# Performance work log

Measured on AMD Instinct MI355X. Metric: run time of the kernel, lower is better.

## Reference

```python
import jax, jax.numpy as jnp
import numpy as np

B, S, DIM, H = 2, 2048, 2048, 16
HD = DIM // H  # 128
ROPE_THETA = 10000.0
NEG = -1e9


def setup_inputs() -> dict:
    key = jax.random.key(0)
    ks = jax.random.split(key, 6)
    x = jax.random.normal(ks[0], (B, S, DIM), dtype=jnp.float32)
    # rotary embedding tables: angle[s, j] = s / theta^(2j/HD), j in [0, HD/2)
    inv_freq = 1.0 / (ROPE_THETA ** (jnp.arange(0, HD, 2, dtype=jnp.float32) / HD))
    angles = jnp.arange(S, dtype=jnp.float32)[:, None] * inv_freq[None, :]  # (S, HD/2)
    freqs_cos = jnp.cos(angles)
    freqs_sin = jnp.sin(angles)
    # causal additive mask (1,1,S,S)
    causal = jnp.tril(jnp.ones((S, S), dtype=jnp.bool_))
    mask = jnp.where(causal, 0.0, NEG).astype(jnp.float32)[None, None]
    sc = 1.0 / np.sqrt(DIM)
    wq = jax.random.normal(ks[1], (DIM, DIM), dtype=jnp.float32) * sc
    wk = jax.random.normal(ks[2], (DIM, DIM), dtype=jnp.float32) * sc
    wv = jax.random.normal(ks[3], (DIM, DIM), dtype=jnp.float32) * sc
    wo = jax.random.normal(ks[4], (DIM, DIM), dtype=jnp.float32) * sc
    return {"x": x, "freqs_cos": freqs_cos, "freqs_sin": freqs_sin,
            "mask": mask, "wq": wq, "wk": wk, "wv": wv, "wo": wo}


def _apply_rope(t, cos, sin):
    # t: (B,S,H,HD); cos/sin: (S, HD/2) -> broadcast (1,S,1,HD/2)
    tr = t[..., ::2]
    ti = t[..., 1::2]
    c = cos[None, :, None, :]
    s = sin[None, :, None, :]
    out_r = tr * c - ti * s
    out_i = tr * s + ti * c
    # interleave back: stack on last axis then flatten -> [r0,i0,r1,i1,...]
    return jnp.stack([out_r, out_i], axis=-1).reshape(t.shape)


def reference(x, freqs_cos, freqs_sin, mask, wq, wk, wv, wo):
    b, s, _ = x.shape
    xq = (x @ wq).reshape(b, s, H, HD)
    xk = (x @ wk).reshape(b, s, H, HD)
    xv = (x @ wv).reshape(b, s, H, HD)
    xq = _apply_rope(xq, freqs_cos, freqs_sin)
    xk = _apply_rope(xk, freqs_cos, freqs_sin)
    # (B,H,S,HD)
    q = jnp.transpose(xq, (0, 2, 1, 3)) * (1.0 / np.sqrt(HD))
    k = jnp.transpose(xk, (0, 2, 1, 3))
    v = jnp.transpose(xv, (0, 2, 1, 3))
    attn = jnp.einsum('bhqd,bhkd->bhqk', q, k) + mask[:, :, :s, :s]
    attn = jax.nn.softmax(attn, axis=-1)
    out = jnp.einsum('bhqk,bhkd->bhqd', attn, v)  # (B,H,S,HD)
    out = jnp.transpose(out, (0, 2, 1, 3)).reshape(b, s, H * HD)
    return out @ wo
```

## Files before the change

kernel.cpp:

```cpp
#include <hip/hip_runtime.h>
#include <hip/hip_bf16.h>
#include <cstdint>
#include <cstddef>

#define BB   2
#define SS   2048
#define DD   2048
#define HH   16
#define HDD  128
#define SEC  8388608

typedef unsigned short u16;
typedef __attribute__((ext_vector_type(8))) short short8;
typedef __attribute__((ext_vector_type(4))) float f32x4;

__device__ __forceinline__ u16 f2bf(float f) {
  union { float f; uint32_t u; } v; v.f = f;
  uint32_t r = v.u + 0x7fffu + ((v.u >> 16) & 1u);
  return (u16)(r >> 16);
}
__device__ __forceinline__ float bf2f(u16 b) {
  union { uint32_t u; float f; } v; v.u = ((uint32_t)b) << 16;
  return v.f;
}

__device__ __forceinline__ void gload16(const u16* g, u16* l) {
  __builtin_amdgcn_global_load_lds(
      (__attribute__((address_space(1))) void*)g,
      (__attribute__((address_space(3))) void*)l, 16, 0, 0);
}

__global__ void k_prep(const float* __restrict__ x,
                       const float* __restrict__ w0, const float* __restrict__ w1,
                       const float* __restrict__ w2, const float* __restrict__ w3,
                       u16* __restrict__ xb, u16* __restrict__ wt) {
  const int z = blockIdx.z;
  if (z == 4) {
    const int id = blockIdx.y * 64 + blockIdx.x;
    const int t = threadIdx.y * 32 + threadIdx.x;
    const size_t base = ((size_t)id * 256 + t) * 2;
    const float4* xv = reinterpret_cast<const float4*>(x);
    uint2* ov = reinterpret_cast<uint2*>(xb);
#pragma unroll
    for (int u = 0; u < 2; ++u) {
      const float4 v = xv[base + u];
      uint2 p;
      p.x = (uint32_t)f2bf(v.x) | ((uint32_t)f2bf(v.y) << 16);
      p.y = (uint32_t)f2bf(v.z) | ((uint32_t)f2bf(v.w) << 16);
      ov[base + u] = p;
    }
    return;
  }
  __shared__ float tls[32][33];
  const float* w = (z == 0) ? w0 : (z == 1) ? w1 : (z == 2) ? w2 : w3;
  u16* o = wt + (size_t)z * (DD * DD);
  const int n0 = blockIdx.x * 32, k0 = blockIdx.y * 32;
  const int tx = threadIdx.x, ty = threadIdx.y;
#pragma unroll
  for (int i = 0; i < 32; i += 8)
    tls[ty + i][tx] = w[(size_t)(k0 + ty + i) * DD + n0 + tx];
  __syncthreads();
#pragma unroll
  for (int i = 0; i < 32; i += 8)
    o[(size_t)(n0 + ty + i) * DD + k0 + tx] = f2bf(tls[tx][ty + i]);
}

template <int MODE>
__global__ __launch_bounds__(256) void k_gemm(const u16* __restrict__ A,
                                              const u16* __restrict__ Bt,
                                              void* __restrict__ out,
                                              const float* __restrict__ fc,
                                              const float* __restrict__ fs) {
  __shared__ __align__(16) u16 As[128 * 32];
  __shared__ __align__(16) u16 Bs[128 * 32];
  const int tid = threadIdx.x;
  const int wave = tid >> 6, lane = tid & 63;
  const int c = lane & 15, g = lane >> 4;
  const int row0 = blockIdx.x * 128, col0 = blockIdx.y * 128;
  const int wm = wave >> 1, wn = wave & 1;
  const int sr = lane >> 2;
  const int sk = (lane & 3) * 8;
  f32x4 acc[4][4] = {};
  for (int k0 = 0; k0 < DD; k0 += 32) {
#pragma unroll
    for (int r = 0; r < 2; ++r) {
      const int chunk = r * 4 + wave;
      const int row = chunk * 16 + sr;
      gload16(A  + (size_t)(row0 + row) * DD + k0 + sk, As + chunk * 512);
      gload16(Bt + (size_t)(col0 + row) * DD + k0 + sk, Bs + chunk * 512);
    }
    __syncthreads();
    short8 a[4], b[4];
#pragma unroll
    for (int i = 0; i < 4; ++i)
      a[i] = *reinterpret_cast<const short8*>(As + (wm * 64 + i * 16 + c) * 32 + g * 8);
#pragma unroll
    for (int j = 0; j < 4; ++j)
      b[j] = *reinterpret_cast<const short8*>(Bs + (wn * 64 + j * 16 + c) * 32 + g * 8);
#pragma unroll
    for (int i = 0; i < 4; ++i)
#pragma unroll
      for (int j = 0; j < 4; ++j)
        acc[i][j] = __builtin_amdgcn_mfma_f32_16x16x32_bf16(a[i], b[j], acc[i][j], 0, 0, 0);
    __syncthreads();
  }
  if (MODE == 0) {
    const int which = col0 >> 11;
    u16* o16 = reinterpret_cast<u16*>(out);
#pragma unroll
    for (int i = 0; i < 4; ++i) {
#pragma unroll
      for (int j = 0; j < 4; ++j) {
        const int mb = row0 + wm * 64 + i * 16 + g * 4;
        const int n  = col0 + wn * 64 + j * 16 + c;
        const int h_ = (n >> 7) & 15, d_ = n & (HDD - 1);
        const int b_ = mb >> 11, s0_ = mb & (SS - 1);
        if (which == 2) {
          ushort4 pk;
          pk.x = f2bf(acc[i][j][0]); pk.y = f2bf(acc[i][j][1]);
          pk.z = f2bf(acc[i][j][2]); pk.w = f2bf(acc[i][j][3]);
          *reinterpret_cast<ushort4*>(
              o16 + 2 * (size_t)SEC + (((size_t)(b_ * HH + h_)) * HDD + d_) * SS + s0_) = pk;
        } else {
          const int p = d_ >> 1;
          const bool ev = (d_ & 1) == 0;
          const float qsc = (which == 0) ? 0.08838834764831845f : 1.0f;
#pragma unroll
          for (int r = 0; r < 4; ++r) {
            const int s_ = s0_ + r;
            const float own = acc[i][j][r];
            const float par = __shfl_xor(own, 1);
            const float cv = fc[s_ * 64 + p], sv = fs[s_ * 64 + p];
            const float ro = ev ? (own * cv - par * sv) : (par * sv + own * cv);
            o16[(size_t)which * SEC + (((size_t)(b_ * HH + h_)) * SS + s_) * HDD + d_] =
                f2bf(ro * qsc);
          }
        }
      }
    }
  } else {
#pragma unroll
    for (int i = 0; i < 4; ++i) {
#pragma unroll
      for (int j = 0; j < 4; ++j) {
        const int mb = row0 + wm * 64 + i * 16 + g * 4;
        const int n  = col0 + wn * 64 + j * 16 + c;
#pragma unroll
        for (int r = 0; r < 4; ++r)
          reinterpret_cast<float*>(out)[(size_t)(mb + r) * DD + n] = acc[i][j][r];
      }
    }
  }
}

__global__ __launch_bounds__(256, 3) void k_attn(const u16* __restrict__ Q,
                                                 const u16* __restrict__ K,
                                                 const u16* __restrict__ Vt,
                                                 u16* __restrict__ O) {
  __shared__ __align__(16) u16 Kt[2][32 * 128];
  __shared__ __align__(16) u16 Vs[2][128 * 32];
  __shared__ __align__(16) u16 Pb[4 * 32 * 40];
  const int tid = threadIdx.x;
  const int wave = tid >> 6, lane = tid & 63;
  const int c = lane & 15, g = lane >> 4;
  const int l = blockIdx.x;
  int qi, bh;
  if (l < 256) { qi = 8 + (l & 7); bh = l >> 3; }
  else         { qi = 7 - ((l - 256) & 7); bh = (l - 256) >> 3; }
  const int q0 = qi * 128;
  const u16* Qp = Q  + (size_t)bh * SS * HDD;
  const u16* Kp = K  + (size_t)bh * SS * HDD;
  const u16* Vp = Vt + (size_t)bh * SS * HDD;
  short8 qf[2][4];
#pragma unroll
  for (int ms = 0; ms < 2; ++ms)
#pragma unroll
    for (int kd = 0; kd < 4; ++kd)
      qf[ms][kd] = *reinterpret_cast<const short8*>(
          Qp + (size_t)(q0 + wave * 32 + ms * 16 + c) * HDD + kd * 32 + g * 8);
  f32x4 acc[2][8] = {};
  float psum[2][4] = {};
  const int ntiles = (qi + 1) * 4;
  u16* pwav = Pb + wave * (32 * 40);
  const int krl = lane >> 4, kcl = lane & 15;
  const int vrl = lane >> 2, vcl = lane & 3;
  auto stage = [&](int t) {
    const int kv0 = t * 32;
    u16* kb = Kt[t & 1];
    u16* vb = Vs[t & 1];
#pragma unroll
    for (int j = 0; j < 2; ++j) {
      const int r0k = (j * 4 + wave) * 4;
      const int rowk = r0k + krl;
      gload16(Kp + (size_t)(kv0 + rowk) * HDD + ((kcl ^ (rowk & 15)) << 3),
              kb + r0k * 128);
      const int r0v = (j * 4 + wave) * 16;
      const int rowv = r0v + vrl;
      gload16(Vp + (size_t)rowv * SS + kv0 + ((vcl ^ (vrl & 3)) << 3),
              vb + r0v * 32);
    }
  };
  stage(0);
  for (int t = 0; t < ntiles; ++t) {
    __syncthreads();
    if (t + 1 < ntiles) stage(t + 1);
    const int kv0 = t * 32;
    const bool active = kv0 <= q0 + wave * 32 + 31;
    if (!active) continue;
    const u16* kb = Kt[t & 1];
    const u16* vv = Vs[t & 1];
    f32x4 s[2][2] = {};
#pragma unroll
    for (int ns = 0; ns < 2; ++ns)
#pragma unroll
      for (int kd = 0; kd < 4; ++kd) {
        const short8 b = *reinterpret_cast<const short8*>(
            kb + (ns * 16 + c) * 128 + (((kd * 4 + g) ^ c) << 3));
        s[0][ns] = __builtin_amdgcn_mfma_f32_16x16x32_bf16(qf[0][kd], b, s[0][ns], 0, 0, 0);
        s[1][ns] = __builtin_amdgcn_mfma_f32_16x16x32_bf16(qf[1][kd], b, s[1][ns], 0, 0, 0);
      }
#pragma unroll
    for (int ms = 0; ms < 2; ++ms) {
      const int qrow = q0 + wave * 32 + ms * 16 + g * 4;
#pragma unroll
      for (int r = 0; r < 4; ++r) {
        u16* pw = pwav + (ms * 16 + g * 4 + r) * 40 + c;
        float rs = 0.f;
#pragma unroll
        for (int ns = 0; ns < 2; ++ns) {
          const bool u = (kv0 + ns * 16 + c) <= (qrow + r);
          const float p = u ? __expf(s[ms][ns][r]) : 0.f;
          rs += p;
          pw[ns * 16] = f2bf(p);
        }
        psum[ms][r] += rs;
      }
    }
    short8 pa[2];
    pa[0] = *reinterpret_cast<const short8*>(pwav + c * 40 + g * 8);
    pa[1] = *reinterpret_cast<const short8*>(pwav + (16 + c) * 40 + g * 8);
#pragma unroll
    for (int nb = 0; nb < 8; ++nb) {
      const short8 vb2 = *reinterpret_cast<const short8*>(
          vv + (nb * 16 + c) * 32 + ((g ^ (c & 3)) << 3));
      acc[0][nb] = __builtin_amdgcn_mfma_f32_16x16x32_bf16(pa[0], vb2, acc[0][nb], 0, 0, 0);
      acc[1][nb] = __builtin_amdgcn_mfma_f32_16x16x32_bf16(pa[1], vb2, acc[1][nb], 0, 0, 0);
    }
  }
  const int b_ = bh >> 4, h_ = bh & 15;
#pragma unroll
  for (int ms = 0; ms < 2; ++ms) {
#pragma unroll
    for (int r = 0; r < 4; ++r) {
      float rs = psum[ms][r];
      rs += __shfl_xor(rs, 1);
      rs += __shfl_xor(rs, 2);
      rs += __shfl_xor(rs, 4);
      rs += __shfl_xor(rs, 8);
      const float inv = 1.f / rs;
      const int s_ = q0 + wave * 32 + ms * 16 + g * 4 + r;
      u16* op = O + ((size_t)(b_ * SS + s_)) * DD + h_ * HDD;
#pragma unroll
      for (int nb = 0; nb < 8; ++nb)
        op[nb * 16 + c] = f2bf(acc[ms][nb][r] * inv);
    }
  }
}

extern "C" void kernel_launch(void* const* d_in, const int* in_sizes, int n_in,
                              void* d_out, int out_size, void* d_ws, size_t ws_size,
                              hipStream_t stream) {
  const float* x  = (const float*)d_in[0];
  const float* fc = (const float*)d_in[1];
  const float* fs = (const float*)d_in[2];
  const float* wq = (const float*)d_in[4];
  const float* wk = (const float*)d_in[5];
  const float* wv = (const float*)d_in[6];
  const float* wo = (const float*)d_in[7];

  u16* ws  = (u16*)d_ws;
  u16* xb  = ws;
  u16* wqt = xb  + 8388608;
  u16* wot = wqt + 3 * 4194304;
  u16* Qb  = wot + 4194304;
  u16* Kb  = Qb  + SEC;
  u16* Vtb = Kb  + SEC;
  u16* ao  = Vtb + SEC;

  k_prep<<<dim3(64, 64, 5), dim3(32, 8), 0, stream>>>(x, wq, wk, wv, wo, xb, wqt);
  k_gemm<0><<<dim3(32, 48), 256, 0, stream>>>(xb, wqt, (void*)Qb, fc, fs);
  k_attn<<<512, 256, 0, stream>>>(Qb, Kb, Vtb, ao);
  k_gemm<1><<<dim3(32, 16), 256, 0, stream>>>(ao, wot, d_out, nullptr, nullptr);
}
```

Before: 437.9 us.

## Replace QKV projection GEMM with 256x256 double-buffered swizzled pipelined kernel

Adds a dedicated QKV GEMM kernel with 256x256 output tiles, 512 threads, and K-step 64. It double-buffers LDS via global_load_lds prefetch two steps ahead, uses an XOR-swizzled LDS layout to avoid bank conflicts, interleaves quarter-tile MFMA blocks with barriers and s_setprio, and remaps block IDs for locality. The goal is higher MFMA utilisation and less global traffic than the old 128x128 single-buffered GEMM. The costs are higher register and LDS pressure and a fragile hand-written waitcnt and barrier schedule.

Measured after the change: 429.3 us. 2.0% less time.

```diff
diff --git a/kernel.cpp b/kernel.cpp
--- a/kernel.cpp
+++ b/kernel.cpp
@@ -9,6 +9,7 @@
 #define HH   16
 #define HDD  128
 #define SEC  8388608
+#define NKT  32
 
 typedef unsigned short u16;
 typedef __attribute__((ext_vector_type(8))) short short8;
@@ -63,6 +64,152 @@
 #pragma unroll
   for (int i = 0; i < 32; i += 8)
     o[(size_t)(n0 + ty + i) * DD + k0 + tx] = f2bf(tls[tx][ty + i]);
+}
+
+__global__ __launch_bounds__(512, 2) void k_qkv(const u16* __restrict__ A,
+                                                const u16* __restrict__ Bt,
+                                                u16* __restrict__ out,
+                                                const float* __restrict__ fc,
+                                                const float* __restrict__ fs) {
+  __shared__ __align__(16) u16 As[2][2][128 * 64];
+  __shared__ __align__(16) u16 Bs[2][2][128 * 64];
+  const int tid = threadIdx.x;
+  const int wave = tid >> 6, lane = tid & 63;
+  const int c = lane & 15, g = lane >> 4;
+  const int wm = wave >> 2, wn = wave & 3;
+  const int x7 = c & 7;
+  const int lb = blockIdx.x;
+  const int wg = (lb & 7) * 48 + (lb >> 3);
+  const int bx = wg / 24, by = wg % 24;
+  const int row0 = bx * 256, col0 = by * 256;
+  const int lr3 = lane >> 3;
+  const int kch = ((lane & 7) ^ lr3) << 3;
+
+  auto stgA = [&](int t, int h) {
+    u16* dst = &As[t & 1][h][0];
+#pragma unroll
+    for (int u = 0; u < 2; ++u)
+      gload16(A + (size_t)(row0 + u * 128 + h * 64 + wave * 8 + lr3) * DD + t * 64 + kch,
+              dst + (u * 64 + wave * 8) * 64);
+  };
+  auto stgB = [&](int t, int h) {
+    u16* dst = &Bs[t & 1][h][0];
+#pragma unroll
+    for (int u = 0; u < 2; ++u)
+      gload16(Bt + (size_t)(col0 + u * 128 + wm * 64 + h * 32 + wn * 8 + lr3) * DD + t * 64 + kch,
+              dst + (u * 64 + wave * 8) * 64);
+  };
+  auto rdA = [&](const u16* bp, int ip, int ks) {
+    return *reinterpret_cast<const short8*>(
+        bp + (wm * 64 + ip * 16 + c) * 64 + ((((ks << 2) | g) ^ x7) << 3));
+  };
+  auto rdB = [&](const u16* bp, int jp, int ks) {
+    return *reinterpret_cast<const short8*>(
+        bp + (wn * 32 + jp * 16 + c) * 64 + ((((ks << 2) | g) ^ x7) << 3));
+  };
+
+  f32x4 acc[8][4] = {};
+  auto quad = [&](short8 (&af)[4][2], short8 (&bf)[2][2], int io, int jo) {
+    __builtin_amdgcn_s_setprio(1);
+#pragma unroll
+    for (int ks = 0; ks < 2; ++ks)
+#pragma unroll
+      for (int ip = 0; ip < 4; ++ip)
+#pragma unroll
+        for (int jp = 0; jp < 2; ++jp)
+          acc[io + ip][jo + jp] = __builtin_amdgcn_mfma_f32_16x16x32_bf16(
+              af[ip][ks], bf[jp][ks], acc[io + ip][jo + jp], 0, 0, 0);
+    __builtin_amdgcn_s_setprio(0);
+  };
+
+  stgA(0, 0); stgB(0, 0); stgB(0, 1); stgA(0, 1);
+  stgA(1, 0); stgB(1, 0); stgB(1, 1); stgA(1, 1);
+  asm volatile("s_waitcnt vmcnt(8)" ::: "memory");
+  __builtin_amdgcn_s_barrier();
+
+  short8 a[4][2], b0[2][2], b1[2][2];
+  for (int t = 0; t < NKT; ++t) {
+    const u16* A0p = &As[t & 1][0][0];
+    const u16* A1p = &As[t & 1][1][0];
+    const u16* B0p = &Bs[t & 1][0][0];
+    const u16* B1p = &Bs[t & 1][1][0];
+    const bool pf = (t + 2 < NKT);
+#pragma unroll
+    for (int ip = 0; ip < 4; ++ip)
+#pragma unroll
+      for (int ks = 0; ks < 2; ++ks)
+        a[ip][ks] = rdA(A0p, ip, ks);
+#pragma unroll
+    for (int jp = 0; jp < 2; ++jp)
+#pragma unroll
+      for (int ks = 0; ks < 2; ++ks)
+        b0[jp][ks] = rdB(B0p, jp, ks);
+    __builtin_amdgcn_s_barrier();
+    asm volatile("s_waitcnt lgkmcnt(0)" ::: "memory");
+    quad(a, b0, 0, 0);
+    __builtin_amdgcn_s_barrier();
+#pragma unroll
+    for (int jp = 0; jp < 2; ++jp)
+#pragma unroll
+      for (int ks = 0; ks < 2; ++ks)
+        b1[jp][ks] = rdB(B1p, jp, ks);
+    if (pf) { stgA(t + 2, 0); stgB(t + 2, 0); }
+    __builtin_amdgcn_s_barrier();
+    asm volatile("s_waitcnt lgkmcnt(0)" ::: "memory");
+    quad(a, b1, 0, 2);
+    __builtin_amdgcn_s_barrier();
+#pragma unroll
+    for (int ip = 0; ip < 4; ++ip)
+#pragma unroll
+      for (int ks = 0; ks < 2; ++ks)
+        a[ip][ks] = rdA(A1p, ip, ks);
+    if (pf) stgB(t + 2, 1);
+    __builtin_amdgcn_s_barrier();
+    asm volatile("s_waitcnt lgkmcnt(0)" ::: "memory");
+    quad(a, b0, 4, 0);
+    __builtin_amdgcn_s_barrier();
+    if (pf) stgA(t + 2, 1);
+    if (t < NKT - 2)
+      asm volatile("s_waitcnt vmcnt(8)" ::: "memory");
+    else if (t == NKT - 2)
+      asm volatile("s_waitcnt vmcnt(0)" ::: "memory");
+    __builtin_amdgcn_s_barrier();
+    quad(a, b1, 4, 2);
+    __builtin_amdgcn_s_barrier();
+  }
+
+  const int which = col0 >> 11;
+#pragma unroll
+  for (int i = 0; i < 8; ++i) {
+    const int mb = row0 + wm * 128 + i * 16 + g * 4;
+    const int b_ = mb >> 11, s0_ = mb & (SS - 1);
+#pragma unroll
+    for (int j = 0; j < 4; ++j) {
+      const int n = col0 + wn * 64 + j * 16 + c;
+      const int h_ = (n >> 7) & 15, d_ = n & (HDD - 1);
+      if (which == 2) {
+        ushort4 pk;
+        pk.x = f2bf(acc[i][j][0]); pk.y = f2bf(acc[i][j][1]);
+        pk.z = f2bf(acc[i][j][2]); pk.w = f2bf(acc[i][j][3]);
+        *reinterpret_cast<ushort4*>(
+            out + 2 * (size_t)SEC + (((size_t)(b_ * HH + h_)) * HDD + d_) * SS + s0_) = pk;
+      } else {
+        const int p = d_ >> 1;
+        const bool ev = (d_ & 1) == 0;
+        const float qsc = (which == 0) ? 0.08838834764831845f : 1.0f;
+#pragma unroll
+        for (int r = 0; r < 4; ++r) {
+          const int s_ = s0_ + r;
+          const float own = acc[i][j][r];
+          const float par = __shfl_xor(own, 1);
+          const float cv = fc[s_ * 64 + p], sv = fs[s_ * 64 + p];
+          const float ro = ev ? (own * cv - par * sv) : (par * sv + own * cv);
+          out[(size_t)which * SEC + (((size_t)(b_ * HH + h_)) * SS + s_) * HDD + d_] =
+              f2bf(ro * qsc);
+        }
+      }
+    }
+  }
 }
 
 template <int MODE>
@@ -104,51 +251,15 @@
         acc[i][j] = __builtin_amdgcn_mfma_f32_16x16x32_bf16(a[i], b[j], acc[i][j], 0, 0, 0);
     __syncthreads();
   }
-  if (MODE == 0) {
-    const int which = col0 >> 11;
-    u16* o16 = reinterpret_cast<u16*>(out);
-#pragma unroll
-    for (int i = 0; i < 4; ++i) {
-#pragma unroll
-      for (int j = 0; j < 4; ++j) {
-        const int mb = row0 + wm * 64 + i * 16 + g * 4;
-        const int n  = col0 + wn * 64 + j * 16 + c;
-        const int h_ = (n >> 7) & 15, d_ = n & (HDD - 1);
-        const int b_ = mb >> 11, s0_ = mb & (SS - 1);
-        if (which == 2) {
-          ushort4 pk;
-          pk.x = f2bf(acc[i][j][0]); pk.y = f2bf(acc[i][j][1]);
-          pk.z = f2bf(acc[i][j][2]); pk.w = f2bf(acc[i][j][3]);
-          *reinterpret_cast<ushort4*>(
-              o16 + 2 * (size_t)SEC + (((size_t)(b_ * HH + h_)) * HDD + d_) * SS + s0_) = pk;
-        } else {
-          const int p = d_ >> 1;
-          const bool ev = (d_ & 1) == 0;
-          const float qsc = (which == 0) ? 0.08838834764831845f : 1.0f;
-#pragma unroll
-          for (int r = 0; r < 4; ++r) {
-            const int s_ = s0_ + r;
-            const float own = acc[i][j][r];
-            const float par = __shfl_xor(own, 1);
-            const float cv = fc[s_ * 64 + p], sv = fs[s_ * 64 + p];
-            const float ro = ev ? (own * cv - par * sv) : (par * sv + own * cv);
-            o16[(size_t)which * SEC + (((size_t)(b_ * HH + h_)) * SS + s_) * HDD + d_] =
-                f2bf(ro * qsc);
-          }
-        }
-      }
-    }
-  } else {
-#pragma unroll
-    for (int i = 0; i < 4; ++i) {
-#pragma unroll
-      for (int j = 0; j < 4; ++j) {
-        const int mb = row0 + wm * 64 + i * 16 + g * 4;
-        const int n  = col0 + wn * 64 + j * 16 + c;
-#pragma unroll
-        for (int r = 0; r < 4; ++r)
-          reinterpret_cast<float*>(out)[(size_t)(mb + r) * DD + n] = acc[i][j][r];
-      }
+#pragma unroll
+  for (int i = 0; i < 4; ++i) {
+#pragma unroll
+    for (int j = 0; j < 4; ++j) {
+      const int mb = row0 + wm * 64 + i * 16 + g * 4;
+      const int n  = col0 + wn * 64 + j * 16 + c;
+#pragma unroll
+      for (int r = 0; r < 4; ++r)
+        reinterpret_cast<float*>(out)[(size_t)(mb + r) * DD + n] = acc[i][j][r];
     }
   }
 }
@@ -288,7 +399,7 @@
   u16* ao  = Vtb + SEC;
 
   k_prep<<<dim3(64, 64, 5), dim3(32, 8), 0, stream>>>(x, wq, wk, wv, wo, xb, wqt);
-  k_gemm<0><<<dim3(32, 48), 256, 0, stream>>>(xb, wqt, (void*)Qb, fc, fs);
+  k_qkv<<<384, 512, 0, stream>>>(xb, wqt, Qb, fc, fs);
   k_attn<<<512, 256, 0, stream>>>(Qb, Kb, Vtb, ao);
   k_gemm<1><<<dim3(32, 16), 256, 0, stream>>>(ao, wot, d_out, nullptr, nullptr);
 }
```
